# Performance work log

Hardware: AMD Instinct MI355X
Metric: run time of the kernel (lower is better)

The kernel has to match this reference:

```python
import jax, jax.numpy as jnp
import numpy as np

NVOC, NIN, NHID = 50257, 1024, 1024
H2 = 2 * NHID  # AttLSTMBlock internal hidden size (cat of h_prev and context)


def setup_inputs() -> dict:
    key = jax.random.key(0)
    ks = jax.random.split(key, 12)
    T, B = 1024, 64
    return {
        "inputs": jax.random.randint(ks[0], (1, B), 0, NVOC),
        "memory_pool": jax.random.normal(ks[1], (T, B, NHID), jnp.float32),
        "h_prev": jax.random.normal(ks[2], (1, B, NHID), jnp.float32),
        "c_prev": jax.random.normal(ks[3], (1, B, H2), jnp.float32),
        "enc_w": jax.random.uniform(ks[4], (NVOC, NIN), jnp.float32, -0.1, 0.1),
        "attWa": jax.random.uniform(ks[5], (NHID, NHID), jnp.float32, -0.1, 0.1),
        "attUa": jax.random.uniform(ks[6], (NHID, NHID), jnp.float32, -0.1, 0.1),
        "attV": jax.random.normal(ks[7], (NHID,), jnp.float32) * 0.1,
        "W_ih": jax.random.normal(ks[8], (NIN, 4 * H2), jnp.float32) * 0.02,
        "W_hh": jax.random.normal(ks[9], (H2, 4 * H2), jnp.float32) * 0.02,
        "b_lstm": jnp.zeros((4 * H2,), jnp.float32),
        "dec_w": jax.random.uniform(ks[10], (NVOC, NHID), jnp.float32, -0.1, 0.1),
        "dec_b": jnp.zeros((NVOC,), jnp.float32),
    }


def reference(inputs, memory_pool, h_prev, c_prev, enc_w, attWa, attUa, attV,
              W_ih, W_hh, b_lstm, dec_w, dec_b):
    # Embedding lookup (dropout = identity in eval mode): [1,B,NIN]
    emb = enc_w[inputs]
    # Bahdanau additive attention: score [T,B], softmax over T (dim=0)
    score = jnp.tanh(h_prev @ attWa + memory_pool @ attUa) @ attV  # [T,B] (h_prev broadcasts over T)
    attWeight = jax.nn.softmax(score, axis=0)
    contextVec = jnp.sum(attWeight[:, :, None] * memory_pool, axis=0)  # [B,NHID]
    att_h = jnp.concatenate([h_prev, contextVec[None]], axis=2)  # [1,B,2*NHID]
    # LSTM cell step with hidden size H2
    gates = emb @ W_ih + att_h @ W_hh + b_lstm  # [1,B,4*H2]
    i, f, g, o = jnp.split(gates, 4, axis=-1)
    ct = jax.nn.sigmoid(f) * c_prev + jax.nn.sigmoid(i) * jnp.tanh(g)
    ht_full = jax.nn.sigmoid(o) * jnp.tanh(ct)
    ht = ht_full[:, :, :NHID]  # slice back to nhid
    # Linear decode
    B = ht.shape[1]
    decoded = (ht.reshape(B, NHID) @ dec_w.T + dec_b).reshape(1, B, NVOC)
    return decoded.squeeze(0), ht, ct
```

## Files before the change

kernel.cpp:

```cpp
#include <hip/hip_runtime.h>

#define T_LEN 1024
#define BATCH 64
#define NHID  1024
#define H2    2048
#define NVOC  50257
#define G4    8192
#define KCAT  3072
#define LS    56

typedef __attribute__((ext_vector_type(4))) float  f4;
typedef __attribute__((ext_vector_type(4))) float  f32x4;
typedef __attribute__((ext_vector_type(8))) __bf16 bf8;
typedef __attribute__((ext_vector_type(4))) __bf16 bf4;

#define GPTR(p) ((const __attribute__((address_space(1))) void*)(p))
#define LPTR(p) ((__attribute__((address_space(3))) void*)(p))

__device__ inline float fast_tanh(float x) {
    float e = __expf(2.0f * x);
    return 1.0f - 2.0f / (e + 1.0f);
}
__device__ inline float fast_sig(float x) {
    return 1.0f / (1.0f + __expf(-x));
}

__global__ __launch_bounds__(256) void cvt_mem(const float* __restrict__ mem,
                                               __bf16* __restrict__ memb) {
    const size_t i = ((size_t)blockIdx.x * 256 + threadIdx.x) * 8;
    f4 a = *(const f4*)(mem + i);
    f4 b = *(const f4*)(mem + i + 4);
    bf8 w;
    w[0] = (__bf16)a[0]; w[1] = (__bf16)a[1]; w[2] = (__bf16)a[2]; w[3] = (__bf16)a[3];
    w[4] = (__bf16)b[0]; w[5] = (__bf16)b[1]; w[6] = (__bf16)b[2]; w[7] = (__bf16)b[3];
    *(bf8*)(memb + i) = w;
}

__global__ __launch_bounds__(256) void transpose_ua(const float* __restrict__ ua,
                                                    __bf16* __restrict__ uaT) {
    __shared__ float tile[64][65];
    const int tid = threadIdx.x;
    const int kb = (blockIdx.x & 15) * 64, nb = (blockIdx.x >> 4) * 64;
#pragma unroll
    for (int i = 0; i < 16; ++i) {
        int idx = tid + 256 * i;
        int kr = idx >> 6, nc = idx & 63;
        tile[kr][nc] = ua[(size_t)(kb + kr) * NHID + nb + nc];
    }
    __syncthreads();
#pragma unroll
    for (int i = 0; i < 16; ++i) {
        int idx = tid + 256 * i;
        int nr = idx >> 6, kc = idx & 63;
        uaT[(size_t)(nb + nr) * NHID + kb + kc] = (__bf16)tile[kc][nr];
    }
}

__global__ void prep_emb_h(const int* __restrict__ inp, const float* __restrict__ enc,
                           const float* __restrict__ h, __bf16* __restrict__ Ag) {
    const int b = blockIdx.x, tid = threadIdx.x;
    const int tok = inp[b];
#pragma unroll
    for (int i = 0; i < 4; ++i) {
        int n = tid + 256 * i;
        Ag[(size_t)b * KCAT + n]        = (__bf16)enc[(size_t)tok * NHID + n];
        Ag[(size_t)b * KCAT + NHID + n] = (__bf16)h[(size_t)b * NHID + n];
    }
}

__global__ __launch_bounds__(256) void small_gemm(
    const __bf16* __restrict__ A, int lda, int K, int k1,
    const float* __restrict__ B1, const float* __restrict__ B2, int ldb,
    float* __restrict__ out, int ldo, int mode) {
    __shared__ __bf16 As[64 * LS];
    __shared__ __bf16 Bs[64 * LS];
    const int tid = threadIdx.x;
    const int lane = tid & 63, wave = tid >> 6;
    const int quad = lane >> 4, l15 = lane & 15;
    const int n0 = blockIdx.x * 64;
    const int ar = tid >> 2, ac = (tid & 3) * 8;

    f32x4 acc[4] = {};

    for (int k0 = 0; k0 < K; k0 += 32) {
        __syncthreads();
        *(bf8*)&As[ar * LS + ac] = *(const bf8*)(A + (size_t)ar * lda + k0 + ac);
#pragma unroll
        for (int j = 0; j < 2; ++j) {
            int idx = tid + 256 * j;
            int kr = idx >> 4, nc = (idx & 15) * 4;
            int kg = k0 + kr;
            const float* src = (kg < k1) ? (B1 + (size_t)kg * ldb)
                                         : (B2 + (size_t)(kg - k1) * ldb);
            f4 v = *(const f4*)(src + n0 + nc);
#pragma unroll
            for (int i = 0; i < 4; ++i) Bs[(nc + i) * LS + kr] = (__bf16)v[i];
        }
        __syncthreads();
        bf8 bfr = *(const bf8*)&Bs[(wave * 16 + l15) * LS + quad * 8];
#pragma unroll
        for (int mi = 0; mi < 4; ++mi) {
            bf8 af = *(const bf8*)&As[(mi * 16 + l15) * LS + quad * 8];
            acc[mi] = __builtin_amdgcn_mfma_f32_16x16x32_bf16(af, bfr, acc[mi], 0, 0, 0);
        }
    }
    const int n = n0 + wave * 16 + l15;
    if (mode == 0) {
#pragma unroll
        for (int mi = 0; mi < 4; ++mi)
#pragma unroll
            for (int r = 0; r < 4; ++r)
                out[(size_t)(mi * 16 + quad * 4 + r) * ldo + n] = acc[mi][r];
    } else {
#pragma unroll
        for (int mi = 0; mi < 4; ++mi)
            *(f4*)&out[(size_t)n * 64 + mi * 16 + quad * 4] = acc[mi];
    }
}

__global__ __launch_bounds__(256) void score_gemm(
    const __bf16* __restrict__ memb, const __bf16* __restrict__ uaT,
    const float* __restrict__ hWaT, const float* __restrict__ attV,
    float* __restrict__ scoreT) {
    __shared__ __bf16 As[128 * 32];
    __shared__ __bf16 Bs[128 * 32];
    const int tid = threadIdx.x;
    const int lane = tid & 63, wave = tid >> 6;
    const int wM = wave >> 1, wN = wave & 1;
    const int quad = lane >> 4, l15 = lane & 15;
    const int bidx = blockIdx.x;
    const int mb = (bidx >> 6) * 8 + (bidx & 7);
    const int nb = (bidx >> 3) & 7;
    const int n0 = nb * 128, m0 = mb * 128;

    const int srow = lane >> 2, scol = (lane & 3) * 8;

    f32x4 acc[4][4] = {};

    for (int k0 = 0; k0 < NHID; k0 += 32) {
        __syncthreads();
#pragma unroll
        for (int j = 0; j < 2; ++j) {
            const int c = wave * 2 + j;
            __builtin_amdgcn_global_load_lds(
                GPTR(memb + (size_t)(m0 + c * 16 + srow) * NHID + k0 + scol),
                LPTR(As + c * 512), 16, 0, 0);
            __builtin_amdgcn_global_load_lds(
                GPTR(uaT + (size_t)(n0 + c * 16 + srow) * NHID + k0 + scol),
                LPTR(Bs + c * 512), 16, 0, 0);
        }
        __syncthreads();
        bf8 af[4], bfr[4];
#pragma unroll
        for (int i = 0; i < 4; ++i)
            af[i] = *(const bf8*)&As[(wM * 64 + i * 16 + l15) * 32 + quad * 8];
#pragma unroll
        for (int i = 0; i < 4; ++i)
            bfr[i] = *(const bf8*)&Bs[(wN * 64 + i * 16 + l15) * 32 + quad * 8];
#pragma unroll
        for (int mi = 0; mi < 4; ++mi)
#pragma unroll
            for (int ni = 0; ni < 4; ++ni)
                acc[mi][ni] = __builtin_amdgcn_mfma_f32_16x16x32_bf16(
                    af[mi], bfr[ni], acc[mi][ni], 0, 0, 0);
    }

    const int tglob = mb * 2 + wM;
#pragma unroll
    for (int mi = 0; mi < 4; ++mi) {
        float rs[4] = {0.f, 0.f, 0.f, 0.f};
#pragma unroll
        for (int ni = 0; ni < 4; ++ni) {
            int n = n0 + wN * 64 + ni * 16 + l15;
            f4 hw = *(const f4*)&hWaT[(size_t)n * 64 + mi * 16 + quad * 4];
            float av = attV[n];
#pragma unroll
            for (int r = 0; r < 4; ++r)
                rs[r] += fast_tanh(acc[mi][ni][r] + hw[r]) * av;
        }
#pragma unroll
        for (int r = 0; r < 4; ++r) {
            float v = rs[r];
            v += __shfl_xor(v, 1); v += __shfl_xor(v, 2);
            v += __shfl_xor(v, 4); v += __shfl_xor(v, 8);
            if (l15 == 0) {
                int b = mi * 16 + quad * 4 + r;
                atomicAdd(&scoreT[b * T_LEN + tglob], v);
            }
        }
    }
}

__global__ __launch_bounds__(256) void score_gemm_f32(
    const float* __restrict__ mem, const __bf16* __restrict__ uaT,
    const float* __restrict__ hWaT, const float* __restrict__ attV,
    float* __restrict__ scoreT) {
    __shared__ __bf16 As[128 * LS];
    __shared__ __bf16 Bs[128 * LS];
    const int tid = threadIdx.x;
    const int lane = tid & 63, wave = tid >> 6;
    const int wM = wave >> 1, wN = wave & 1;
    const int quad = lane >> 4, l15 = lane & 15;
    const int mb = blockIdx.x >> 3, nb = blockIdx.x & 7;
    const int n0 = nb * 128;
    const int arow = tid >> 1, ahalf = (tid & 1) * 16;
    const float*  aptr = mem + (size_t)(mb * 128 + arow) * NHID + ahalf;
    const __bf16* bptr = uaT + (size_t)(n0 + arow) * NHID + ahalf;
    f4  ga[4];
    bf8 gb[2];
#pragma unroll
    for (int j = 0; j < 4; ++j) ga[j] = *(const f4*)(aptr + 4 * j);
#pragma unroll
    for (int j = 0; j < 2; ++j) gb[j] = *(const bf8*)(bptr + 8 * j);
    f32x4 acc[4][4] = {};
    for (int k0 = 0; k0 < NHID; k0 += 32) {
        __syncthreads();
#pragma unroll
        for (int j = 0; j < 4; ++j) {
            bf4 w;
            w[0] = (__bf16)ga[j][0]; w[1] = (__bf16)ga[j][1];
            w[2] = (__bf16)ga[j][2]; w[3] = (__bf16)ga[j][3];
            *(bf4*)&As[arow * LS + ahalf + 4 * j] = w;
        }
#pragma unroll
        for (int j = 0; j < 2; ++j) *(bf8*)&Bs[arow * LS + ahalf + 8 * j] = gb[j];
        __syncthreads();
        if (k0 + 32 < NHID) {
#pragma unroll
            for (int j = 0; j < 4; ++j) ga[j] = *(const f4*)(aptr + k0 + 32 + 4 * j);
#pragma unroll
            for (int j = 0; j < 2; ++j) gb[j] = *(const bf8*)(bptr + k0 + 32 + 8 * j);
        }
        bf8 af[4], bfr[4];
#pragma unroll
        for (int i = 0; i < 4; ++i)
            af[i] = *(const bf8*)&As[(wM * 64 + i * 16 + l15) * LS + quad * 8];
#pragma unroll
        for (int i = 0; i < 4; ++i)
            bfr[i] = *(const bf8*)&Bs[(wN * 64 + i * 16 + l15) * LS + quad * 8];
#pragma unroll
        for (int mi = 0; mi < 4; ++mi)
#pragma unroll
            for (int ni = 0; ni < 4; ++ni)
                acc[mi][ni] = __builtin_amdgcn_mfma_f32_16x16x32_bf16(
                    af[mi], bfr[ni], acc[mi][ni], 0, 0, 0);
    }
    const int tglob = mb * 2 + wM;
#pragma unroll
    for (int mi = 0; mi < 4; ++mi) {
        float rs[4] = {0.f, 0.f, 0.f, 0.f};
#pragma unroll
        for (int ni = 0; ni < 4; ++ni) {
            int n = n0 + wN * 64 + ni * 16 + l15;
            f4 hw = *(const f4*)&hWaT[(size_t)n * 64 + mi * 16 + quad * 4];
            float av = attV[n];
#pragma unroll
            for (int r = 0; r < 4; ++r)
                rs[r] += fast_tanh(acc[mi][ni][r] + hw[r]) * av;
        }
#pragma unroll
        for (int r = 0; r < 4; ++r) {
            float v = rs[r];
            v += __shfl_xor(v, 1); v += __shfl_xor(v, 2);
            v += __shfl_xor(v, 4); v += __shfl_xor(v, 8);
            if (l15 == 0) {
                int b = mi * 16 + quad * 4 + r;
                atomicAdd(&scoreT[b * T_LEN + tglob], v);
            }
        }
    }
}

__global__ void softmax_k(const float* __restrict__ scoreT, float* __restrict__ wts) {
    const int b = blockIdx.x, tid = threadIdx.x;
    const int lane = tid & 63, wave = tid >> 6;
    __shared__ float red[4];
    __shared__ float red2[4];
    float s[4];
    float mx = -1e30f;
#pragma unroll
    for (int i = 0; i < 4; ++i) {
        s[i] = scoreT[b * T_LEN + tid + 256 * i];
        mx = fmaxf(mx, s[i]);
    }
#pragma unroll
    for (int o = 1; o < 64; o <<= 1) mx = fmaxf(mx, __shfl_xor(mx, o));
    if (lane == 0) red[wave] = mx;
    __syncthreads();
    mx = fmaxf(fmaxf(red[0], red[1]), fmaxf(red[2], red[3]));
    float e[4], sum = 0.f;
#pragma unroll
    for (int i = 0; i < 4; ++i) { e[i] = __expf(s[i] - mx); sum += e[i]; }
#pragma unroll
    for (int o = 1; o < 64; o <<= 1) sum += __shfl_xor(sum, o);
    if (lane == 0) red2[wave] = sum;
    __syncthreads();
    sum = red2[0] + red2[1] + red2[2] + red2[3];
    float inv = 1.0f / sum;
#pragma unroll
    for (int i = 0; i < 4; ++i) wts[b * T_LEN + tid + 256 * i] = e[i] * inv;
}

__global__ void context_k(const float* __restrict__ wts, const float* __restrict__ mem,
                          float* __restrict__ ctx) {
    const int b = blockIdx.x >> 3, tc = blockIdx.x & 7;
    const int n4 = threadIdx.x * 4;
    f4 acc = {0.f, 0.f, 0.f, 0.f};
    const int t0 = tc * 128;
    for (int t = t0; t < t0 + 128; ++t) {
        float w = wts[b * T_LEN + t];
        f4 m = *(const f4*)(mem + ((size_t)t * BATCH + b) * NHID + n4);
        acc += w * m;
    }
#pragma unroll
    for (int i = 0; i < 4; ++i) atomicAdd(&ctx[(size_t)b * NHID + n4 + i], acc[i]);
}

__global__ void ctx_cvt(const float* __restrict__ ctx, __bf16* __restrict__ Ag) {
    const int b = blockIdx.x, tid = threadIdx.x;
#pragma unroll
    for (int i = 0; i < 4; ++i) {
        int n = tid + 256 * i;
        Ag[(size_t)b * KCAT + H2 + n] = (__bf16)ctx[(size_t)b * NHID + n];
    }
}

__global__ void lstm_k(const float* __restrict__ gates, const float* __restrict__ bl,
                       const float* __restrict__ cprev, float* __restrict__ out_ct,
                       float* __restrict__ out_ht, __bf16* __restrict__ htb) {
    const int idx = blockIdx.x * 256 + threadIdx.x;
    const int b = idx >> 11, k = idx & 2047;
    float gi = gates[(size_t)b * G4 + k]          + bl[k];
    float gf = gates[(size_t)b * G4 + H2 + k]     + bl[H2 + k];
    float gg = gates[(size_t)b * G4 + 2 * H2 + k] + bl[2 * H2 + k];
    float go = gates[(size_t)b * G4 + 3 * H2 + k] + bl[3 * H2 + k];
    float ct = fast_sig(gf) * cprev[idx] + fast_sig(gi) * fast_tanh(gg);
    float ht = fast_sig(go) * fast_tanh(ct);
    out_ct[idx] = ct;
    if (k < NHID) {
        out_ht[(size_t)b * NHID + k] = ht;
        htb[(size_t)b * NHID + k]    = (__bf16)ht;
    }
}

__global__ __launch_bounds__(256) void dec_gemm(
    const __bf16* __restrict__ htb, const float* __restrict__ dw,
    const float* __restrict__ db, float* __restrict__ outd) {
    __shared__ __bf16 As[64 * LS];
    __shared__ __bf16 Bs[128 * LS];
    const int tid = threadIdx.x;
    const int lane = tid & 63, wave = tid >> 6;
    const int quad = lane >> 4, l15 = lane & 15;
    const int n0 = blockIdx.x * 128;
    const int ar = tid >> 2, ac = (tid & 3) * 8;
    const int br = tid >> 1, bc = (tid & 1) * 16;
    const int vrow = n0 + br;

    f32x4 acc[4][2] = {};

    for (int k0 = 0; k0 < NHID; k0 += 32) {
        __syncthreads();
        *(bf8*)&As[ar * LS + ac] = *(const bf8*)(htb + (size_t)ar * NHID + k0 + ac);
#pragma unroll
        for (int j = 0; j < 4; ++j) {
            f4 v = {0.f, 0.f, 0.f, 0.f};
            if (vrow < NVOC) v = *(const f4*)(dw + (size_t)vrow * NHID + k0 + bc + 4 * j);
            bf4 w;
            w[0] = (__bf16)v[0]; w[1] = (__bf16)v[1];
            w[2] = (__bf16)v[2]; w[3] = (__bf16)v[3];
            *(bf4*)&Bs[br * LS + bc + 4 * j] = w;
        }
        __syncthreads();
#pragma unroll
        for (int ni = 0; ni < 2; ++ni) {
            bf8 bfr = *(const bf8*)&Bs[(wave * 32 + ni * 16 + l15) * LS + quad * 8];
#pragma unroll
            for (int mi = 0; mi < 4; ++mi) {
                bf8 af = *(const bf8*)&As[(mi * 16 + l15) * LS + quad * 8];
                acc[mi][ni] = __builtin_amdgcn_mfma_f32_16x16x32_bf16(af, bfr, acc[mi][ni], 0, 0, 0);
            }
        }
    }
#pragma unroll
    for (int ni = 0; ni < 2; ++ni) {
        int n = n0 + wave * 32 + ni * 16 + l15;
        if (n < NVOC) {
            float bb = db[n];
#pragma unroll
            for (int mi = 0; mi < 4; ++mi)
#pragma unroll
                for (int r = 0; r < 4; ++r)
                    outd[(size_t)(mi * 16 + quad * 4 + r) * NVOC + n] = acc[mi][ni][r] + bb;
        }
    }
}

extern "C" void kernel_launch(void* const* d_in, const int* in_sizes, int n_in,
                              void* d_out, int out_size, void* d_ws, size_t ws_size,
                              hipStream_t stream) {
    (void)in_sizes; (void)n_in; (void)out_size;
    const int*   inp   = (const int*)d_in[0];
    const float* mem   = (const float*)d_in[1];
    const float* hprev = (const float*)d_in[2];
    const float* cprev = (const float*)d_in[3];
    const float* encw  = (const float*)d_in[4];
    const float* attWa = (const float*)d_in[5];
    const float* attUa = (const float*)d_in[6];
    const float* attV  = (const float*)d_in[7];
    const float* Wih   = (const float*)d_in[8];
    const float* Whh   = (const float*)d_in[9];
    const float* blstm = (const float*)d_in[10];
    const float* decw  = (const float*)d_in[11];
    const float* decb  = (const float*)d_in[12];

    char* ws = (char*)d_ws;
    float*  scoreT = (float*)(ws);
    float*  wts    = (float*)(ws + 262144);
    float*  hWaT   = (float*)(ws + 524288);
    float*  ctx    = (float*)(ws + 786432);
    float*  gates  = (float*)(ws + 1048576);
    __bf16* Ag     = (__bf16*)(ws + 3145728);
    __bf16* htb    = (__bf16*)(ws + 3538944);
    __bf16* uaT    = (__bf16*)(ws + 3670016);
    __bf16* memb   = (__bf16*)(ws + 5767168);
    const size_t ws_need = 5767168 + (size_t)T_LEN * BATCH * NHID * 2;

    float* outdec = (float*)d_out;
    float* outht  = outdec + (size_t)BATCH * NVOC;
    float* outct  = outht + BATCH * NHID;

    hipMemsetAsync(scoreT, 0, 262144, stream);
    hipMemsetAsync(ctx, 0, 262144, stream);
    hipLaunchKernelGGL(transpose_ua, dim3(256), dim3(256), 0, stream, attUa, uaT);
    hipLaunchKernelGGL(prep_emb_h, dim3(64), dim3(256), 0, stream, inp, encw, hprev, Ag);
    hipLaunchKernelGGL(small_gemm, dim3(16), dim3(256), 0, stream,
                       Ag + NHID, KCAT, NHID, NHID, attWa, attWa, NHID, hWaT, 64, 1);
    if (ws_size >= ws_need) {
        hipLaunchKernelGGL(cvt_mem, dim3(32768), dim3(256), 0, stream, mem, memb);
        hipLaunchKernelGGL(score_gemm, dim3(4096), dim3(256), 0, stream,
                           memb, uaT, hWaT, attV, scoreT);
    } else {
        hipLaunchKernelGGL(score_gemm_f32, dim3(4096), dim3(256), 0, stream,
                           mem, uaT, hWaT, attV, scoreT);
    }
    hipLaunchKernelGGL(softmax_k, dim3(64), dim3(256), 0, stream, scoreT, wts);
    hipLaunchKernelGGL(context_k, dim3(512), dim3(256), 0, stream, wts, mem, ctx);
    hipLaunchKernelGGL(ctx_cvt, dim3(64), dim3(256), 0, stream, ctx, Ag);
    hipLaunchKernelGGL(small_gemm, dim3(128), dim3(256), 0, stream,
                       Ag, KCAT, KCAT, NHID, Wih, Whh, G4, gates, G4, 0);
    hipLaunchKernelGGL(lstm_k, dim3(512), dim3(256), 0, stream,
                       gates, blstm, cprev, outct, outht, htb);
    hipLaunchKernelGGL(dec_gemm, dim3((NVOC + 127) / 128), dim3(256), 0, stream,
                       htb, decw, decb, outdec);
}
```

Before: 1.176 ms.

## Double-buffer score GEMM, prefetch registers in small/dec GEMMs, read bf16 memory in context

The score GEMM now double-buffers its LDS tiles: the global-to-LDS loads for the next K step are issued before the current step's MFMAs, and the column offsets are XOR-swizzled to reduce LDS bank conflicts. small_gemm and dec_gemm prefetch the next K tile into registers while the current tile is being computed. The context reduction reads the bf16 copy of memory_pool instead of the fp32 one, which halves the bytes read but lowers input precision there. The double buffer doubles LDS use in score_gemm, which may reduce occupancy.

```diff
diff --git a/kernel.cpp b/kernel.cpp
--- a/kernel.cpp
+++ b/kernel.cpp
@@ -79,24 +79,38 @@
     const int quad = lane >> 4, l15 = lane & 15;
     const int n0 = blockIdx.x * 64;
     const int ar = tid >> 2, ac = (tid & 3) * 8;
+    const int kr = tid >> 4, nc = (tid & 15) * 4;
 
     f32x4 acc[4] = {};
+    bf8 pa = *(const bf8*)(A + (size_t)ar * lda + ac);
+    f4 pv[2];
+#pragma unroll
+    for (int j = 0; j < 2; ++j) {
+        int kg = kr + 16 * j;
+        const float* src = (kg < k1) ? (B1 + (size_t)kg * ldb)
+                                     : (B2 + (size_t)(kg - k1) * ldb);
+        pv[j] = *(const f4*)(src + n0 + nc);
+    }
 
     for (int k0 = 0; k0 < K; k0 += 32) {
         __syncthreads();
-        *(bf8*)&As[ar * LS + ac] = *(const bf8*)(A + (size_t)ar * lda + k0 + ac);
-#pragma unroll
-        for (int j = 0; j < 2; ++j) {
-            int idx = tid + 256 * j;
-            int kr = idx >> 4, nc = (idx & 15) * 4;
-            int kg = k0 + kr;
-            const float* src = (kg < k1) ? (B1 + (size_t)kg * ldb)
-                                         : (B2 + (size_t)(kg - k1) * ldb);
-            f4 v = *(const f4*)(src + n0 + nc);
-#pragma unroll
-            for (int i = 0; i < 4; ++i) Bs[(nc + i) * LS + kr] = (__bf16)v[i];
-        }
-        __syncthreads();
+        *(bf8*)&As[ar * LS + ac] = pa;
+#pragma unroll
+        for (int j = 0; j < 2; ++j)
+#pragma unroll
+            for (int i = 0; i < 4; ++i)
+                Bs[(nc + i) * LS + kr + 16 * j] = (__bf16)pv[j][i];
+        __syncthreads();
+        if (k0 + 32 < K) {
+            pa = *(const bf8*)(A + (size_t)ar * lda + k0 + 32 + ac);
+#pragma unroll
+            for (int j = 0; j < 2; ++j) {
+                int kg = k0 + 32 + kr + 16 * j;
+                const float* src = (kg < k1) ? (B1 + (size_t)kg * ldb)
+                                             : (B2 + (size_t)(kg - k1) * ldb);
+                pv[j] = *(const f4*)(src + n0 + nc);
+            }
+        }
         bf8 bfr = *(const bf8*)&Bs[(wave * 16 + l15) * LS + quad * 8];
 #pragma unroll
         for (int mi = 0; mi < 4; ++mi) {
@@ -122,8 +136,8 @@
     const __bf16* __restrict__ memb, const __bf16* __restrict__ uaT,
     const float* __restrict__ hWaT, const float* __restrict__ attV,
     float* __restrict__ scoreT) {
-    __shared__ __bf16 As[128 * 32];
-    __shared__ __bf16 Bs[128 * 32];
+    __shared__ __bf16 As[2][128 * 32];
+    __shared__ __bf16 Bs[2][128 * 32];
     const int tid = threadIdx.x;
     const int lane = tid & 63, wave = tid >> 6;
     const int wM = wave >> 1, wN = wave & 1;
@@ -133,30 +147,44 @@
     const int nb = (bidx >> 3) & 7;
     const int n0 = nb * 128, m0 = mb * 128;
 
-    const int srow = lane >> 2, scol = (lane & 3) * 8;
+    const int srow = lane >> 2;
+    const int scol = ((lane & 3) ^ ((lane >> 3) & 3)) * 8;
+    const __bf16* aSrc = memb + (size_t)(m0 + srow) * NHID + scol;
+    const __bf16* bSrc = uaT + (size_t)(n0 + srow) * NHID + scol;
+    const int rslot = (quad ^ ((l15 >> 1) & 3)) * 8;
 
     f32x4 acc[4][4] = {};
 
-    for (int k0 = 0; k0 < NHID; k0 += 32) {
-        __syncthreads();
-#pragma unroll
-        for (int j = 0; j < 2; ++j) {
-            const int c = wave * 2 + j;
-            __builtin_amdgcn_global_load_lds(
-                GPTR(memb + (size_t)(m0 + c * 16 + srow) * NHID + k0 + scol),
-                LPTR(As + c * 512), 16, 0, 0);
-            __builtin_amdgcn_global_load_lds(
-                GPTR(uaT + (size_t)(n0 + c * 16 + srow) * NHID + k0 + scol),
-                LPTR(Bs + c * 512), 16, 0, 0);
-        }
-        __syncthreads();
+#pragma unroll
+    for (int j = 0; j < 2; ++j) {
+        const int c = wave * 2 + j;
+        __builtin_amdgcn_global_load_lds(GPTR(aSrc + (size_t)c * 16 * NHID),
+                                         LPTR(&As[0][c * 512]), 16, 0, 0);
+        __builtin_amdgcn_global_load_lds(GPTR(bSrc + (size_t)c * 16 * NHID),
+                                         LPTR(&Bs[0][c * 512]), 16, 0, 0);
+    }
+
+    for (int it = 0; it < 32; ++it) {
+        const int cur = it & 1, nxt = cur ^ 1;
+        __syncthreads();
+        if (it + 1 < 32) {
+            const int k = (it + 1) * 32;
+#pragma unroll
+            for (int j = 0; j < 2; ++j) {
+                const int c = wave * 2 + j;
+                __builtin_amdgcn_global_load_lds(GPTR(aSrc + (size_t)c * 16 * NHID + k),
+                                                 LPTR(&As[nxt][c * 512]), 16, 0, 0);
+                __builtin_amdgcn_global_load_lds(GPTR(bSrc + (size_t)c * 16 * NHID + k),
+                                                 LPTR(&Bs[nxt][c * 512]), 16, 0, 0);
+            }
+        }
         bf8 af[4], bfr[4];
 #pragma unroll
         for (int i = 0; i < 4; ++i)
-            af[i] = *(const bf8*)&As[(wM * 64 + i * 16 + l15) * 32 + quad * 8];
+            af[i] = *(const bf8*)&As[cur][(wM * 64 + i * 16 + l15) * 32 + rslot];
 #pragma unroll
         for (int i = 0; i < 4; ++i)
-            bfr[i] = *(const bf8*)&Bs[(wN * 64 + i * 16 + l15) * 32 + quad * 8];
+            bfr[i] = *(const bf8*)&Bs[cur][(wN * 64 + i * 16 + l15) * 32 + rslot];
 #pragma unroll
         for (int mi = 0; mi < 4; ++mi)
 #pragma unroll
@@ -301,6 +329,22 @@
     for (int i = 0; i < 4; ++i) wts[b * T_LEN + tid + 256 * i] = e[i] * inv;
 }
 
+__global__ void context_kb(const float* __restrict__ wts, const __bf16* __restrict__ memb,
+                           float* __restrict__ ctx) {
+    const int b = blockIdx.x >> 3, tc = blockIdx.x & 7;
+    const int n4 = threadIdx.x * 4;
+    f4 acc = {0.f, 0.f, 0.f, 0.f};
+    const int t0 = tc * 128;
+    for (int t = t0; t < t0 + 128; ++t) {
+        float w = wts[b * T_LEN + t];
+        bf4 m = *(const bf4*)(memb + ((size_t)t * BATCH + b) * NHID + n4);
+#pragma unroll
+        for (int i = 0; i < 4; ++i) acc[i] += w * (float)m[i];
+    }
+#pragma unroll
+    for (int i = 0; i < 4; ++i) atomicAdd(&ctx[(size_t)b * NHID + n4 + i], acc[i]);
+}
+
 __global__ void context_k(const float* __restrict__ wts, const float* __restrict__ mem,
                           float* __restrict__ ctx) {
     const int b = blockIdx.x >> 3, tc = blockIdx.x & 7;
@@ -355,22 +399,32 @@
     const int ar = tid >> 2, ac = (tid & 3) * 8;
     const int br = tid >> 1, bc = (tid & 1) * 16;
     const int vrow = n0 + br;
+    const bool vok = vrow < NVOC;
 
     f32x4 acc[4][2] = {};
+    bf8 pa = *(const bf8*)(htb + (size_t)ar * NHID + ac);
+    f4 pv[4] = {};
+#pragma unroll
+    for (int j = 0; j < 4; ++j)
+        if (vok) pv[j] = *(const f4*)(dw + (size_t)vrow * NHID + bc + 4 * j);
 
     for (int k0 = 0; k0 < NHID; k0 += 32) {
         __syncthreads();
-        *(bf8*)&As[ar * LS + ac] = *(const bf8*)(htb + (size_t)ar * NHID + k0 + ac);
+        *(bf8*)&As[ar * LS + ac] = pa;
 #pragma unroll
         for (int j = 0; j < 4; ++j) {
-            f4 v = {0.f, 0.f, 0.f, 0.f};
-            if (vrow < NVOC) v = *(const f4*)(dw + (size_t)vrow * NHID + k0 + bc + 4 * j);
             bf4 w;
-            w[0] = (__bf16)v[0]; w[1] = (__bf16)v[1];
-            w[2] = (__bf16)v[2]; w[3] = (__bf16)v[3];
+            w[0] = (__bf16)pv[j][0]; w[1] = (__bf16)pv[j][1];
+            w[2] = (__bf16)pv[j][2]; w[3] = (__bf16)pv[j][3];
             *(bf4*)&Bs[br * LS + bc + 4 * j] = w;
         }
         __syncthreads();
+        if (k0 + 32 < NHID) {
+            pa = *(const bf8*)(htb + (size_t)ar * NHID + k0 + 32 + ac);
+#pragma unroll
+            for (int j = 0; j < 4; ++j)
+                if (vok) pv[j] = *(const f4*)(dw + (size_t)vrow * NHID + k0 + 32 + bc + 4 * j);
+        }
 #pragma unroll
         for (int ni = 0; ni < 2; ++ni) {
             bf8 bfr = *(const bf8*)&Bs[(wave * 32 + ni * 16 + l15) * LS + quad * 8];
@@ -435,7 +489,8 @@
     hipLaunchKernelGGL(prep_emb_h, dim3(64), dim3(256), 0, stream, inp, encw, hprev, Ag);
     hipLaunchKernelGGL(small_gemm, dim3(16), dim3(256), 0, stream,
                        Ag + NHID, KCAT, NHID, NHID, attWa, attWa, NHID, hWaT, 64, 1);
-    if (ws_size >= ws_need) {
+    const bool big_ws = ws_size >= ws_need;
+    if (big_ws) {
         hipLaunchKernelGGL(cvt_mem, dim3(32768), dim3(256), 0, stream, mem, memb);
         hipLaunchKernelGGL(score_gemm, dim3(4096), dim3(256), 0, stream,
                            memb, uaT, hWaT, attV, scoreT);
@@ -444,7 +499,11 @@
                            mem, uaT, hWaT, attV, scoreT);
     }
     hipLaunchKernelGGL(softmax_k, dim3(64), dim3(256), 0, stream, scoreT, wts);
-    hipLaunchKernelGGL(context_k, dim3(512), dim3(256), 0, stream, wts, mem, ctx);
+    if (big_ws) {
+        hipLaunchKernelGGL(context_kb, dim3(512), dim3(256), 0, stream, wts, memb, ctx);
+    } else {
+        hipLaunchKernelGGL(context_k, dim3(512), dim3(256), 0, stream, wts, mem, ctx);
+    }
     hipLaunchKernelGGL(ctx_cvt, dim3(64), dim3(256), 0, stream, ctx, Ag);
     hipLaunchKernelGGL(small_gemm, dim3(128), dim3(256), 0, stream,
                        Ag, KCAT, KCAT, NHID, Wih, Whh, G4, gates, G4, 0);
```

New measurement: 1.047 ms. -10.9%, faster.
